# Optimization experiments

Measured on AMD Instinct MI355X. Metric: run time of the kernel, lower is better.

The kernel has to match this reference:

```python
import jax, jax.numpy as jnp
import numpy as np

R = 131072   # rays
S = 128      # existing samples per ray (existing_bins has S+1 edges)
N_NEW = 64   # new importance samples per ray
HIST_PAD = 1e-5   # NeuSSampler builds PDFSampler(histogram_padding=1e-5)
EPS = 1e-5


def setup_inputs() -> dict:
    key = jax.random.key(0)
    k1, k2, k3, k4 = jax.random.split(key, 4)
    weights = jax.random.uniform(k1, (R, S, 1), dtype=jnp.float32)
    # existing spacing bins must be sorted in [0,1] along the sample axis
    existing_bins = jnp.sort(jax.random.uniform(k2, (R, S + 1), dtype=jnp.float32), axis=-1)
    nears = 0.05 + 0.5 * jax.random.uniform(k3, (R, 1), dtype=jnp.float32)
    fars = nears + 1.0 + 3.0 * jax.random.uniform(k4, (R, 1), dtype=jnp.float32)
    return {"weights": weights, "existing_bins": existing_bins,
            "nears": nears, "fars": fars, "num_samples": N_NEW}


def reference(weights, existing_bins, nears, fars, num_samples):
    # PDFSampler.generate_ray_samples core (eval mode, include_original=False)
    num_bins = num_samples + 1
    w = weights[..., 0] + HIST_PAD                      # [R, S]
    w_sum = jnp.sum(w, axis=-1, keepdims=True)          # [R, 1]
    padding = jax.nn.relu(EPS - w_sum)
    w = w + padding / w.shape[-1]
    w_sum = w_sum + padding
    pdf = w / w_sum                                     # [R, S]
    cdf = jnp.minimum(jnp.ones_like(pdf), jnp.cumsum(pdf, axis=-1))
    cdf = jnp.concatenate([jnp.zeros_like(cdf[..., :1]), cdf], axis=-1)  # [R, S+1]

    # deterministic mid-bin query points (non-stratified branch)
    u = jnp.linspace(0.0, 1.0 - 1.0 / num_bins, num_bins, dtype=cdf.dtype)
    u = u + 1.0 / (2 * num_bins)
    u = jnp.broadcast_to(u, (*cdf.shape[:-1], num_bins))  # [R, num_bins]

    # inverse-CDF: per-ray binary search + gather + linear interp
    inds = jax.vmap(lambda c, q: jnp.searchsorted(c, q, side='right'))(cdf, u)
    last = existing_bins.shape[-1] - 1
    below = jnp.clip(inds - 1, 0, last)
    above = jnp.clip(inds, 0, last)
    cdf_g0 = jnp.take_along_axis(cdf, below, axis=-1)
    bins_g0 = jnp.take_along_axis(existing_bins, below, axis=-1)
    cdf_g1 = jnp.take_along_axis(cdf, above, axis=-1)
    bins_g1 = jnp.take_along_axis(existing_bins, above, axis=-1)
    t = jnp.clip(jnp.nan_to_num((u - cdf_g0) / (cdf_g1 - cdf_g0), nan=0.0,
                                posinf=0.0, neginf=0.0), 0.0, 1.0)
    bins = bins_g0 + t * (bins_g1 - bins_g0)            # [R, num_bins]
    bins = jax.lax.stop_gradient(bins)                  # torch: bins.detach()

    # spacing_to_euclidean_fn for UniformSampler: x*s_far + (1-x)*s_near
    euclidean_bins = bins * fars + (1.0 - bins) * nears  # [R, num_bins]
    return euclidean_bins
```

## Files before the change

kernel.cpp:

```cpp
#include <hip/hip_runtime.h>


#define DPP_FADD(x, ctrl, rmask)                                             \
    ((x) + __int_as_float(__builtin_amdgcn_update_dpp(                       \
               0, __float_as_int(x), (ctrl), (rmask), 0xf, true)))

__global__ __launch_bounds__(256) void neus_sampler_kernel(
    const float* __restrict__ weights,
    const float* __restrict__ bins_g,
    const float* __restrict__ nears,
    const float* __restrict__ fars,
    float* __restrict__ out,
    int R)
{
    constexpr int S  = 128;
    constexpr int NB = 65;
    constexpr float HPAD = 1e-5f;

    const int lane = threadIdx.x & 63;
    const int ray  = blockIdx.x * 4 + (threadIdx.x >> 6);
    if (ray >= R) return;
    const int uray = __builtin_amdgcn_readfirstlane(ray);

    const float2 wpair =
        reinterpret_cast<const float2*>(weights + (size_t)uray * S)[lane];
    const float* brow = bins_g + (size_t)uray * (S + 1);
    const float2 bpair = reinterpret_cast<const float2*>(brow)[lane];
    const float b_last = brow[S];

    const float w1 = wpair.y + HPAD;
    float ps = (wpair.x + HPAD) + w1;

    ps = DPP_FADD(ps, 0x111, 0xf);
    ps = DPP_FADD(ps, 0x112, 0xf);
    ps = DPP_FADD(ps, 0x114, 0xf);
    ps = DPP_FADD(ps, 0x118, 0xf);
    ps = DPP_FADD(ps, 0x142, 0xa);
    ps = DPP_FADD(ps, 0x143, 0xc);

    const float total =
        __int_as_float(__builtin_amdgcn_readlane(__float_as_int(ps), 63));
    const float padding = fmaxf(1e-5f - total, 0.0f);
    const float padc    = padding * (1.0f / S);
    const float inv     = __builtin_amdgcn_rcpf(total + padding);

    const float c_hi  = fminf(1.0f, fmaf((float)(2 * lane + 2), padc, ps) * inv);
    const float c_mid = fminf(1.0f, fmaf((float)(2 * lane + 1), padc, ps - w1) * inv);
    float c_lo = __shfl_up(c_hi, 1, 64);
    if (lane == 0) c_lo = 0.0f;
    float b2 = __shfl_down(bpair.x, 1, 64);
    if (lane == 63) b2 = b_last;

    const float nearv = nears[uray];
    const float farv  = fars[uray];
    const float fmn   = farv - nearv;
    float* orow = out + (size_t)uray * NB;

    auto jf = [](float c) -> int {
        int j = (int)ceilf(fmaf(65.0f, c, -0.5f));
        return j < 0 ? 0 : (j > NB ? NB : j);
    };

    const int j0 = jf(c_lo);
    const int j2 = (lane == 63) ? NB : jf(c_hi);
    int j1 = jf(c_mid);
    j1 = j1 < j0 ? j0 : (j1 > j2 ? j2 : j1);

    if (j1 > j0) {
        const float r  = __builtin_amdgcn_rcpf(c_mid - c_lo);
        const float dt = r * (1.0f / 65.0f);
        const float bd = bpair.y - bpair.x;
        float u = (float)(2 * j0 + 1) * (1.0f / 130.0f);
        float t = (u - c_lo) * r;
        for (int j = j0; j < j1; ++j) {
            const float tc = fminf(fmaxf(t, 0.0f), 1.0f);
            orow[j] = fmaf(fmaf(tc, bd, bpair.x), fmn, nearv);
            t += dt;
        }
    }
    if (j2 > j1) {
        const float r  = __builtin_amdgcn_rcpf(c_hi - c_mid);
        const float dt = r * (1.0f / 65.0f);
        const float bd = b2 - bpair.y;
        float u = (float)(2 * j1 + 1) * (1.0f / 130.0f);
        float t = (u - c_mid) * r;
        for (int j = j1; j < j2; ++j) {
            const float tc = fminf(fmaxf(t, 0.0f), 1.0f);
            orow[j] = fmaf(fmaf(tc, bd, bpair.y), fmn, nearv);
            t += dt;
        }
    }
}

extern "C" void kernel_launch(void* const* d_in, const int* in_sizes, int n_in,
                              void* d_out, int out_size, void* d_ws, size_t ws_size,
                              hipStream_t stream) {
    const float* weights = (const float*)d_in[0];
    const float* ebins   = (const float*)d_in[1];
    const float* nears   = (const float*)d_in[2];
    const float* fars    = (const float*)d_in[3];
    float* out = (float*)d_out;
    const int R = in_sizes[0] / 128;
    const int blocks = (R + 3) / 4;
    hipLaunchKernelGGL(neus_sampler_kernel, dim3(blocks), dim3(256), 0, stream,
                       weights, ebins, nears, fars, out, R);
}
```

Before: 163.4 us.

## Stage per-sample interpolation params in LDS for coalesced output stores

Each lane now writes the interpolation parameters (cdf start, reciprocal width, scaled bin base, scaled bin delta) for every output index it owns into a per-wave shared-memory array. After a wait on LDS, each lane reads back one entry and writes one output, so the global stores become contiguous per wave instead of scattered variable-length per-lane loops. This relies on intra-wave LDS visibility without a barrier and adds LDS traffic. Folding near/far into the stored parameters also changes the floating-point rounding slightly.

```diff
diff --git a/kernel.cpp b/kernel.cpp
--- a/kernel.cpp
+++ b/kernel.cpp
@@ -17,8 +17,11 @@
     constexpr int NB = 65;
     constexpr float HPAD = 1e-5f;
 
+    __shared__ float4 pay[4][NB];
+
     const int lane = threadIdx.x & 63;
-    const int ray  = blockIdx.x * 4 + (threadIdx.x >> 6);
+    const int wv   = threadIdx.x >> 6;
+    const int ray  = blockIdx.x * 4 + wv;
     if (ray >= R) return;
     const int uray = __builtin_amdgcn_readfirstlane(ray);
 
@@ -54,7 +57,6 @@
     const float nearv = nears[uray];
     const float farv  = fars[uray];
     const float fmn   = farv - nearv;
-    float* orow = out + (size_t)uray * NB;
 
     auto jf = [](float c) -> int {
         int j = (int)ceilf(fmaf(65.0f, c, -0.5f));
@@ -66,29 +68,38 @@
     int j1 = jf(c_mid);
     j1 = j1 < j0 ? j0 : (j1 > j2 ? j2 : j1);
 
+    float4* const wp = &pay[wv][0];
+
     if (j1 > j0) {
-        const float r  = __builtin_amdgcn_rcpf(c_mid - c_lo);
-        const float dt = r * (1.0f / 65.0f);
-        const float bd = bpair.y - bpair.x;
-        float u = (float)(2 * j0 + 1) * (1.0f / 130.0f);
-        float t = (u - c_lo) * r;
-        for (int j = j0; j < j1; ++j) {
-            const float tc = fminf(fmaxf(t, 0.0f), 1.0f);
-            orow[j] = fmaf(fmaf(tc, bd, bpair.x), fmn, nearv);
-            t += dt;
-        }
+        const float r = __builtin_amdgcn_rcpf(c_mid - c_lo);
+        const float4 v = make_float4(c_lo, r,
+                                     fmaf(bpair.x, fmn, nearv),
+                                     (bpair.y - bpair.x) * fmn);
+        for (int j = j0; j < j1; ++j) wp[j] = v;
     }
     if (j2 > j1) {
-        const float r  = __builtin_amdgcn_rcpf(c_hi - c_mid);
-        const float dt = r * (1.0f / 65.0f);
-        const float bd = b2 - bpair.y;
-        float u = (float)(2 * j1 + 1) * (1.0f / 130.0f);
-        float t = (u - c_mid) * r;
-        for (int j = j1; j < j2; ++j) {
-            const float tc = fminf(fmaxf(t, 0.0f), 1.0f);
-            orow[j] = fmaf(fmaf(tc, bd, bpair.y), fmn, nearv);
-            t += dt;
-        }
+        const float r = __builtin_amdgcn_rcpf(c_hi - c_mid);
+        const float4 v = make_float4(c_mid, r,
+                                     fmaf(bpair.y, fmn, nearv),
+                                     (b2 - bpair.y) * fmn);
+        for (int j = j1; j < j2; ++j) wp[j] = v;
+    }
+
+    asm volatile("s_waitcnt lgkmcnt(0)" ::: "memory");
+
+    float* const orow = out + (size_t)uray * NB;
+    {
+        const float4 p  = wp[lane];
+        const float  u  = (float)(2 * lane + 1) * (1.0f / 130.0f);
+        const float  t  = (u - p.x) * p.y;
+        const float  tc = fminf(fmaxf(t, 0.0f), 1.0f);
+        orow[lane] = fmaf(tc, p.w, p.z);
+    }
+    if (lane == 0) {
+        const float4 p  = wp[64];
+        const float  t  = (129.0f / 130.0f - p.x) * p.y;
+        const float  tc = fminf(fmaxf(t, 0.0f), 1.0f);
+        orow[64] = fmaf(tc, p.w, p.z);
     }
 }
 
```

New measurement: 163.3 us. No clear change (-0.1%).

## Process two rays per wavefront and coalesce output writes via LDS scatter

Applied to the files above, without the earlier changes.

Each wavefront now handles two rays, one per 32-lane half, and each lane loads float4s covering four CDF bins. Instead of every lane writing its own variable-length run of outputs with scattered stores, lanes write per-sample interpolation parameters into shared memory. Each output sample then reads those parameters and computes its value, so global stores become coalesced one per lane. This trades irregular global writes for LDS traffic and an intra-wave LDS dependency enforced only with s_waitcnt, and it uses more registers for four segments per lane.

```diff
diff --git a/kernel.cpp b/kernel.cpp
--- a/kernel.cpp
+++ b/kernel.cpp
@@ -17,78 +17,107 @@
     constexpr int NB = 65;
     constexpr float HPAD = 1e-5f;
 
+    __shared__ float4 pay[4][2][NB];
+
     const int lane = threadIdx.x & 63;
-    const int ray  = blockIdx.x * 4 + (threadIdx.x >> 6);
-    if (ray >= R) return;
-    const int uray = __builtin_amdgcn_readfirstlane(ray);
+    const int wv   = threadIdx.x >> 6;
+    const int q    = lane & 31;
+    const int h    = lane >> 5;
+    const int ray0 = (blockIdx.x * 4 + wv) * 2;
+    if (ray0 >= R) return;
+    const int uray = __builtin_amdgcn_readfirstlane(ray0);
+    const int rayB = (uray + 1 < R) ? uray + 1 : uray;
+    const bool haveB = (uray + 1 < R);
 
-    const float2 wpair =
-        reinterpret_cast<const float2*>(weights + (size_t)uray * S)[lane];
-    const float* brow = bins_g + (size_t)uray * (S + 1);
-    const float2 bpair = reinterpret_cast<const float2*>(brow)[lane];
-    const float b_last = brow[S];
+    const float4 wq = *reinterpret_cast<const float4*>(
+        weights + (size_t)uray * S + (size_t)(h ? (rayB - uray) : 0) * S + q * 4);
+    const float4 bq = *reinterpret_cast<const float4*>(
+        bins_g + (size_t)(h ? rayB : uray) * (S + 1) + q * 4);
+    const float bLA = bins_g[(size_t)uray * (S + 1) + S];
+    const float bLB = bins_g[(size_t)rayB * (S + 1) + S];
+    const float nA = nears[uray], nB = nears[rayB];
+    const float fA = fars[uray],  fB = fars[rayB];
 
-    const float w1 = wpair.y + HPAD;
-    float ps = (wpair.x + HPAD) + w1;
+    const float w0 = wq.x + HPAD, w1 = wq.y + HPAD;
+    const float w2 = wq.z + HPAD, w3 = wq.w + HPAD;
+    const float s1 = w0, s2 = s1 + w1, s3 = s2 + w2, s4 = s3 + w3;
 
+    float ps = s4;
     ps = DPP_FADD(ps, 0x111, 0xf);
     ps = DPP_FADD(ps, 0x112, 0xf);
     ps = DPP_FADD(ps, 0x114, 0xf);
     ps = DPP_FADD(ps, 0x118, 0xf);
     ps = DPP_FADD(ps, 0x142, 0xa);
-    ps = DPP_FADD(ps, 0x143, 0xc);
 
-    const float total =
-        __int_as_float(__builtin_amdgcn_readlane(__float_as_int(ps), 63));
+    const float tA = __int_as_float(__builtin_amdgcn_readlane(__float_as_int(ps), 31));
+    const float tB = __int_as_float(__builtin_amdgcn_readlane(__float_as_int(ps), 63));
+    const float total = h ? tB : tA;
+
     const float padding = fmaxf(1e-5f - total, 0.0f);
     const float padc    = padding * (1.0f / S);
     const float inv     = __builtin_amdgcn_rcpf(total + padding);
 
-    const float c_hi  = fminf(1.0f, fmaf((float)(2 * lane + 2), padc, ps) * inv);
-    const float c_mid = fminf(1.0f, fmaf((float)(2 * lane + 1), padc, ps - w1) * inv);
-    float c_lo = __shfl_up(c_hi, 1, 64);
-    if (lane == 0) c_lo = 0.0f;
-    float b2 = __shfl_down(bpair.x, 1, 64);
-    if (lane == 63) b2 = b_last;
+    const float excl = ps - s4;
+    const float g = (float)(4 * q);
+    float e[5];
+    e[4] = fminf(1.0f, fmaf(g + 4.0f, padc, ps) * inv);
+    e[1] = fminf(1.0f, fmaf(g + 1.0f, padc, excl + s1) * inv);
+    e[2] = fminf(1.0f, fmaf(g + 2.0f, padc, excl + s2) * inv);
+    e[3] = fminf(1.0f, fmaf(g + 3.0f, padc, excl + s3) * inv);
+    const float elo = __shfl_up(e[4], 1, 32);
+    e[0] = (q == 0) ? 0.0f : elo;
 
-    const float nearv = nears[uray];
-    const float farv  = fars[uray];
-    const float fmn   = farv - nearv;
-    float* orow = out + (size_t)uray * NB;
+    float bb[5];
+    bb[0] = bq.x; bb[1] = bq.y; bb[2] = bq.z; bb[3] = bq.w;
+    const float bn = __shfl_down(bq.x, 1, 32);
+    bb[4] = (q == 31) ? (h ? bLB : bLA) : bn;
+
+    const float nearv = h ? nB : nA;
+    const float fmn   = (h ? fB : fA) - nearv;
 
     auto jf = [](float c) -> int {
         int j = (int)ceilf(fmaf(65.0f, c, -0.5f));
         return j < 0 ? 0 : (j > NB ? NB : j);
     };
 
-    const int j0 = jf(c_lo);
-    const int j2 = (lane == 63) ? NB : jf(c_hi);
-    int j1 = jf(c_mid);
-    j1 = j1 < j0 ? j0 : (j1 > j2 ? j2 : j1);
+    int J[5];
+    J[0] = jf(e[0]);
+    J[4] = (q == 31) ? NB : jf(e[4]);
+    J[1] = jf(e[1]); J[2] = jf(e[2]); J[3] = jf(e[3]);
+    J[1] = J[1] < J[0] ? J[0] : (J[1] > J[4] ? J[4] : J[1]);
+    J[2] = J[2] < J[1] ? J[1] : (J[2] > J[4] ? J[4] : J[2]);
+    J[3] = J[3] < J[2] ? J[2] : (J[3] > J[4] ? J[4] : J[3]);
 
-    if (j1 > j0) {
-        const float r  = __builtin_amdgcn_rcpf(c_mid - c_lo);
-        const float dt = r * (1.0f / 65.0f);
-        const float bd = bpair.y - bpair.x;
-        float u = (float)(2 * j0 + 1) * (1.0f / 130.0f);
-        float t = (u - c_lo) * r;
-        for (int j = j0; j < j1; ++j) {
-            const float tc = fminf(fmaxf(t, 0.0f), 1.0f);
-            orow[j] = fmaf(fmaf(tc, bd, bpair.x), fmn, nearv);
-            t += dt;
+    float4* const wp = &pay[wv][h][0];
+
+#pragma unroll
+    for (int i = 0; i < 4; ++i) {
+        if (J[i + 1] > J[i]) {
+            const float r = __builtin_amdgcn_rcpf(e[i + 1] - e[i]);
+            const float4 v = make_float4(e[i], r,
+                                         fmaf(bb[i], fmn, nearv),
+                                         (bb[i + 1] - bb[i]) * fmn);
+            for (int j = J[i]; j < J[i + 1]; ++j) wp[j] = v;
         }
     }
-    if (j2 > j1) {
-        const float r  = __builtin_amdgcn_rcpf(c_hi - c_mid);
-        const float dt = r * (1.0f / 65.0f);
-        const float bd = b2 - bpair.y;
-        float u = (float)(2 * j1 + 1) * (1.0f / 130.0f);
-        float t = (u - c_mid) * r;
-        for (int j = j1; j < j2; ++j) {
-            const float tc = fminf(fmaxf(t, 0.0f), 1.0f);
-            orow[j] = fmaf(fmaf(tc, bd, bpair.y), fmn, nearv);
-            t += dt;
-        }
+
+    asm volatile("s_waitcnt lgkmcnt(0)" ::: "memory");
+
+    const float u = (float)(2 * lane + 1) * (1.0f / 130.0f);
+    {
+        const float4 p  = pay[wv][0][lane];
+        const float  tc = fminf(fmaxf((u - p.x) * p.y, 0.0f), 1.0f);
+        out[(size_t)uray * NB + lane] = fmaf(tc, p.w, p.z);
+    }
+    if (haveB) {
+        const float4 p  = pay[wv][1][lane];
+        const float  tc = fminf(fmaxf((u - p.x) * p.y, 0.0f), 1.0f);
+        out[(size_t)rayB * NB + lane] = fmaf(tc, p.w, p.z);
+    }
+    if (lane < 2 && (lane == 0 || haveB)) {
+        const float4 p  = pay[wv][lane][64];
+        const float  tc = fminf(fmaxf((129.0f / 130.0f - p.x) * p.y, 0.0f), 1.0f);
+        out[(size_t)(uray + lane) * NB + 64] = fmaf(tc, p.w, p.z);
     }
 }
 
@@ -101,7 +130,7 @@
     const float* fars    = (const float*)d_in[3];
     float* out = (float*)d_out;
     const int R = in_sizes[0] / 128;
-    const int blocks = (R + 3) / 4;
+    const int blocks = (R + 7) / 8;
     hipLaunchKernelGGL(neus_sampler_kernel, dim3(blocks), dim3(256), 0, stream,
                        weights, ebins, nears, fars, out, R);
 }
```

After: 163.7 us. No clear change (+0.2%).
